# Kernel tuning notes

Measured on AMD Instinct MI355X. Metric: run time of the kernel, lower is better.

## Reference

```python
import jax, jax.numpy as jnp
import numpy as np

N_HEAD, DIM, D_K, D_V = 16, 1024, 64, 64
B, L = 4, 2048


def setup_inputs() -> dict:
    key = jax.random.key(0)
    ks = jax.random.split(key, 8)
    def xavier(k, shape, fan_in, fan_out):
        std = float(np.sqrt(2.0 / (fan_in + fan_out)))
        return jax.random.normal(k, shape, dtype=jnp.float32) * std
    return {
        "q": jax.random.normal(ks[0], (B, L, DIM), dtype=jnp.float32),
        "k": jax.random.normal(ks[1], (B, L, DIM), dtype=jnp.float32),
        "v": jax.random.normal(ks[2], (B, L, DIM), dtype=jnp.float32),
        "w_q": xavier(ks[3], (N_HEAD, DIM, D_K), DIM, D_K),
        "w_k": xavier(ks[4], (N_HEAD, DIM, D_K), DIM, D_K),
        "w_v": xavier(ks[5], (N_HEAD, DIM, D_V), DIM, D_V),
        "proj_w": xavier(ks[6], (DIM, N_HEAD * D_V), N_HEAD * D_V, DIM),
        "proj_b": jnp.zeros((DIM,), dtype=jnp.float32),
    }


def reference(q, k, v, w_q, w_k, w_v, proj_w, proj_b):
    batch, len_q, dim = q.shape
    # NOTE: original scales by sqrt(dim) (model dim), not sqrt(d_k)
    scale = jnp.asarray(np.sqrt(dim), dtype=q.dtype)
    # per-head projections: [h, b, q, dk]
    qh = jnp.einsum('bqd,hdk->hbqk', q, w_q)
    kh = jnp.einsum('bsd,hdk->hbsk', k, w_k)
    vh = jnp.einsum('bsd,hdv->hbsv', v, w_v)
    scores = jnp.einsum('hbqk,hbsk->hbqs', qh, kh) / scale
    attn = jax.nn.softmax(scores, axis=-1)
    out = jnp.einsum('hbqs,hbsv->hbqv', attn, vh)
    # concat heads along last dim: [b, q, h*dv] (head-major order, matching torch.cat(split))
    out = jnp.transpose(out, (1, 2, 0, 3)).reshape(batch, len_q, -1)
    # output projection (dropout is identity at eval)
    return out @ proj_w.T + proj_b
```

## Files before the change

kernel.cpp:

```cpp
#include <hip/hip_runtime.h>
#include <hip/hip_bf16.h>
#include <stdint.h>

#define NH 16
#define DM 1024
#define DKV 64
#define BB 4
#define LL 2048
#define MT (BB*LL)
#define NT (LL/64)

typedef __bf16 bf16;
typedef __bf16 bf16x8 __attribute__((ext_vector_type(8)));
typedef float f32x4 __attribute__((ext_vector_type(4)));
typedef float f32x16 __attribute__((ext_vector_type(16)));
typedef unsigned int u32x2 __attribute__((ext_vector_type(2)));
typedef unsigned int u32x4 __attribute__((ext_vector_type(4)));

__device__ __forceinline__ void gload_lds16(const void* g, void* l) {
  __builtin_amdgcn_global_load_lds(
      (const __attribute__((address_space(1))) unsigned int*)g,
      (__attribute__((address_space(3))) unsigned int*)l, 16, 0, 0);
}

__device__ __forceinline__ unsigned short bfbits(float x) {
  bf16 b = (bf16)x;
  return __builtin_bit_cast(unsigned short, b);
}

__device__ __forceinline__ float fast_exp2(float x) {
#if defined(__has_builtin)
#if __has_builtin(__builtin_amdgcn_exp2f)
  return __builtin_amdgcn_exp2f(x);
#else
  float r; asm("v_exp_f32 %0, %1" : "=v"(r) : "v"(x)); return r;
#endif
#else
  float r; asm("v_exp_f32 %0, %1" : "=v"(r) : "v"(x)); return r;
#endif
}

#if defined(__has_builtin)
#if __has_builtin(__builtin_amdgcn_permlane32_swap)
#define HAVE_PLSWAP 1
#endif
#endif

__device__ __forceinline__ u32x2 plswap(unsigned int a, unsigned int b, int hi) {
#ifdef HAVE_PLSWAP
  auto rr = __builtin_amdgcn_permlane32_swap(a, b, false, false);
  u32x2 r; r.x = rr[0]; r.y = rr[1];
  return r;
#else
  unsigned int pa = (unsigned int)__shfl_xor((int)a, 32);
  unsigned int pb_ = (unsigned int)__shfl_xor((int)b, 32);
  u32x2 r;
  r.x = hi ? pb_ : a;
  r.y = hi ? b : pa;
  return r;
#endif
}

__device__ __forceinline__ bf16x8 pack8(const f32x4& lo, const f32x4& hi2) {
  u32x4 u;
  u.x = (unsigned int)bfbits(lo[0]) | ((unsigned int)bfbits(lo[1]) << 16);
  u.y = (unsigned int)bfbits(lo[2]) | ((unsigned int)bfbits(lo[3]) << 16);
  u.z = (unsigned int)bfbits(hi2[0]) | ((unsigned int)bfbits(hi2[1]) << 16);
  u.w = (unsigned int)bfbits(hi2[2]) | ((unsigned int)bfbits(hi2[3]) << 16);
  return __builtin_bit_cast(bf16x8, u);
}

__global__ __launch_bounds__(256) void prep_w(const float* __restrict__ w0, const float* __restrict__ w1,
                                              const float* __restrict__ w2, const float* __restrict__ pw,
                                              bf16* __restrict__ o0, bf16* __restrict__ o1,
                                              bf16* __restrict__ o2, bf16* __restrict__ Wp) {
  __shared__ float t[64][65];
  if (blockIdx.z < 3) {
    const float* w = blockIdx.z == 0 ? w0 : (blockIdx.z == 1 ? w1 : w2);
    bf16* o = blockIdx.z == 0 ? o0 : (blockIdx.z == 1 ? o1 : o2);
    int h = blockIdx.y, d0 = blockIdx.x * 64;
    const float* src = w + ((size_t)h * DM + d0) * DKV;
    for (int i = threadIdx.x; i < 64 * 64; i += 256) {
      int r = i >> 6, c = i & 63;
      t[r][c] = src[(size_t)r * DKV + c];
    }
    __syncthreads();
    for (int i = threadIdx.x; i < 64 * 64; i += 256) {
      int kk = i >> 6, d = i & 63;
      o[((size_t)(h * 64 + kk)) * DM + d0 + d] = (bf16)t[d][kk];
    }
  } else {
    int base = ((blockIdx.y * 16 + blockIdx.x) * 256 + threadIdx.x) * 2;
#pragma unroll
    for (int e = 0; e < 2; ++e) {
      int i = base + e;
      const float4* p = (const float4*)pw + (size_t)i * 2;
      float4 a = p[0], b = p[1];
      bf16x8 r;
      r[0] = (bf16)a.x; r[1] = (bf16)a.y; r[2] = (bf16)a.z; r[3] = (bf16)a.w;
      r[4] = (bf16)b.x; r[5] = (bf16)b.y; r[6] = (bf16)b.z; r[7] = (bf16)b.w;
      *((bf16x8*)Wp + i) = r;
    }
  }
}

__global__ __launch_bounds__(256) void gemm_qkv(const float* __restrict__ Qf, const float* __restrict__ Kf,
                                                const float* __restrict__ Vf, const bf16* __restrict__ Wqt,
                                                const bf16* __restrict__ Wkt, const bf16* __restrict__ Wvt,
                                                bf16* __restrict__ QH, bf16* __restrict__ KH,
                                                bf16* __restrict__ VT) {
  __shared__ float sAf[128 * 64];
  __shared__ bf16 sB[128 * 64];
  const int bid = blockIdx.x;
  const int xcd = bid & 7;
  const int j   = bid >> 3;
  const int nb  = j & 7;
  const int t   = j >> 3;
  const int mb  = xcd + 8 * (t & 7);
  const int mode = t >> 3;
  const float* A = mode == 0 ? Qf : (mode == 1 ? Kf : Vf);
  const bf16* Bt = mode == 0 ? Wqt : (mode == 1 ? Wkt : Wvt);
  const int tid = threadIdx.x;
  const int w = tid >> 6, l = tid & 63;
  const int c = l & 15, g4 = l >> 4;
  const int wm = w >> 1, wn = w & 1;
  const int m0 = mb * 128, n0 = nb * 128;

  f32x4 acc[4][4] = {};
  for (int kt = 0; kt < 1024; kt += 64) {
#pragma unroll
    for (int jj = 0; jj < 8; ++jj) {
      int gi = jj * 256 + tid;
      int row = gi >> 4, slot = gi & 15;
      int sg = slot ^ (row & 15);
      gload_lds16(A + (size_t)(m0 + row) * 1024 + kt + sg * 4,
                  (char*)sAf + (jj * 256 + w * 64) * 16);
    }
#pragma unroll
    for (int i = 0; i < 4; ++i) {
      int blk = i * 4 + w;
      int row = blk * 8 + (l >> 3);
      int g = (l & 7) ^ (row & 7);
      gload_lds16(Bt + ((size_t)(n0 + row)) * 1024 + kt + g * 8, (char*)sB + blk * 1024);
    }
    __syncthreads();
#pragma unroll
    for (int ks = 0; ks < 2; ++ks) {
      bf16x8 af[4], bfr[4];
#pragma unroll
      for (int x = 0; x < 4; ++x) {
        int ar = wm * 64 + x * 16 + c;
        int p0 = ks * 8 + g4 * 2;
        int s0 = p0 ^ (ar & 15), s1 = (p0 + 1) ^ (ar & 15);
        f32x4 lo = *(const f32x4*)((const char*)sAf + ar * 256 + s0 * 16);
        f32x4 hi2 = *(const f32x4*)((const char*)sAf + ar * 256 + s1 * 16);
        af[x] = pack8(lo, hi2);
        int br = wn * 64 + x * 16 + c;
        bfr[x] = *(const bf16x8*)((const char*)sB + br * 128 + (((ks * 4 + g4) ^ (br & 7)) * 16));
      }
#pragma unroll
      for (int x = 0; x < 4; ++x)
#pragma unroll
        for (int y = 0; y < 4; ++y)
          acc[x][y] = __builtin_amdgcn_mfma_f32_16x16x32_bf16(af[x], bfr[y], acc[x][y], 0, 0, 0);
    }
    __syncthreads();
  }

  const int mm = m0 + wm * 64, nn = n0 + wn * 64;
  if (mode < 2) {
    bf16* O = mode == 0 ? QH : KH;
    const float s = (mode == 0) ? 0.03125f * 1.44269504088896f : 1.0f;
#pragma unroll
    for (int x = 0; x < 4; ++x)
#pragma unroll
      for (int y = 0; y < 4; ++y)
#pragma unroll
        for (int r = 0; r < 4; ++r) {
          int m = mm + x * 16 + g4 * 4 + r;
          int n = nn + y * 16 + c;
          O[(size_t)m * 1024 + n] = (bf16)(acc[x][y][r] * s);
        }
  } else {
    bf16* O = VT;
#pragma unroll
    for (int x = 0; x < 4; ++x)
#pragma unroll
      for (int y = 0; y < 4; ++y) {
        int mb2 = mm + x * 16 + g4 * 4;
        int n = nn + y * 16 + c;
        int bb2 = mb2 >> 11, sidx = mb2 & 2047;
        int hh2 = n >> 6, dv = n & 63;
        unsigned int u0 = bfbits(acc[x][y][0]) | ((unsigned int)bfbits(acc[x][y][1]) << 16);
        unsigned int u1 = bfbits(acc[x][y][2]) | ((unsigned int)bfbits(acc[x][y][3]) << 16);
        *(uint2*)(O + ((size_t)((hh2 * 4 + bb2) * 64 + dv)) * LL + sidx) = make_uint2(u0, u1);
      }
  }
}

__global__ __launch_bounds__(256) void gemm_proj(const bf16* __restrict__ A, const bf16* __restrict__ Bt,
                                                 float* __restrict__ Out, const float* __restrict__ bias) {
  __shared__ bf16 sA[128 * 64];
  __shared__ bf16 sB[128 * 64];
  const int tid = threadIdx.x;
  const int w = tid >> 6, l = tid & 63;
  const int c = l & 15, g4 = l >> 4;
  const int wm = w >> 1, wn = w & 1;
  const int m0 = blockIdx.y * 128, n0 = blockIdx.x * 128;

  f32x4 acc[4][4] = {};
  for (int kt = 0; kt < 1024; kt += 64) {
#pragma unroll
    for (int i = 0; i < 4; ++i) {
      int blk = i * 4 + w;
      int row = blk * 8 + (l >> 3);
      int g = (l & 7) ^ (row & 7);
      gload_lds16(A + ((size_t)(m0 + row)) * 1024 + kt + g * 8, (char*)sA + blk * 1024);
      gload_lds16(Bt + ((size_t)(n0 + row)) * 1024 + kt + g * 8, (char*)sB + blk * 1024);
    }
    __syncthreads();
#pragma unroll
    for (int ks = 0; ks < 2; ++ks) {
      bf16x8 af[4], bfr[4];
#pragma unroll
      for (int x = 0; x < 4; ++x) {
        int ar = wm * 64 + x * 16 + c;
        af[x] = *(const bf16x8*)((const char*)sA + ar * 128 + (((ks * 4 + g4) ^ (ar & 7)) * 16));
        int br = wn * 64 + x * 16 + c;
        bfr[x] = *(const bf16x8*)((const char*)sB + br * 128 + (((ks * 4 + g4) ^ (br & 7)) * 16));
      }
#pragma unroll
      for (int x = 0; x < 4; ++x)
#pragma unroll
        for (int y = 0; y < 4; ++y)
          acc[x][y] = __builtin_amdgcn_mfma_f32_16x16x32_bf16(af[x], bfr[y], acc[x][y], 0, 0, 0);
    }
    __syncthreads();
  }

  const int mm = m0 + wm * 64, nn = n0 + wn * 64;
#pragma unroll
  for (int x = 0; x < 4; ++x)
#pragma unroll
    for (int y = 0; y < 4; ++y)
#pragma unroll
      for (int r = 0; r < 4; ++r) {
        int m = mm + x * 16 + g4 * 4 + r;
        int n = nn + y * 16 + c;
        Out[(size_t)m * 1024 + n] = acc[x][y][r] + bias[n];
      }
}

__global__ __launch_bounds__(256, 2) void attn_kernel(const bf16* __restrict__ qh,
                                                      const bf16* __restrict__ kh,
                                                      const bf16* __restrict__ vt,
                                                      bf16* __restrict__ o) {
  __shared__ bf16 sK[4][64 * 64];
  __shared__ bf16 sV[4][64 * 64];
  const int tid = threadIdx.x, w = tid >> 6, l = tid & 63;
  const int c = l & 31, hi = l >> 5;
  const int bh = blockIdx.x, b = bh & 3, h = bh >> 2;
  const int q0 = blockIdx.y * 256 + w * 64;

  const bf16* qbase = qh + ((size_t)(b * LL)) * DM + h * 64;
  const bf16* kbase = kh + ((size_t)(b * LL)) * DM + h * 64;
  const bf16* vbase = vt + ((size_t)((h * 4 + b) * 64)) * LL;

  bf16x8 qfA[4], qfB[4];
#pragma unroll
  for (int ks = 0; ks < 4; ++ks) {
    qfA[ks] = *(const bf16x8*)(qbase + (size_t)(q0 + c) * DM + ks * 16 + hi * 8);
    qfB[ks] = *(const bf16x8*)(qbase + (size_t)(q0 + 32 + c) * DM + ks * 16 + hi * 8);
  }

  bf16x8 onesf;
#pragma unroll
  for (int i = 0; i < 8; ++i) onesf[i] = (bf16)1.0f;

  f32x16 oA0 = {}, oA1 = {}, oB0 = {}, oB1 = {};
  f32x16 lAa = {}, lBa = {};

  auto STAGE = [&](int bufi, int kv0) {
#pragma unroll
    for (int j = 0; j < 2; ++j) {
      int gi = w * 128 + j * 64 + l;
      int row = gi >> 3;
      int g = (gi & 7) ^ (row & 7);
      gload_lds16(kbase + (size_t)(kv0 + row) * DM + g * 8,
                  (char*)sK[bufi] + (w * 128 + j * 64) * 16);
      gload_lds16(vbase + (size_t)row * LL + kv0 + g * 8,
                  (char*)sV[bufi] + (w * 128 + j * 64) * 16);
    }
  };

  auto EXPPACK = [&](f32x16& st0, f32x16& st1, bf16x8* pb) {
#pragma unroll
    for (int r = 0; r < 16; ++r) st0[r] = fast_exp2(st0[r]);
#pragma unroll
    for (int r = 0; r < 16; ++r) st1[r] = fast_exp2(st1[r]);
#pragma unroll
    for (int t = 0; t < 2; ++t) {
      const f32x16& st = t ? st1 : st0;
      unsigned int u[4][2];
#pragma unroll
      for (int g2 = 0; g2 < 4; ++g2) {
        u[g2][0] = (unsigned int)bfbits(st[4 * g2 + 0]) | ((unsigned int)bfbits(st[4 * g2 + 1]) << 16);
        u[g2][1] = (unsigned int)bfbits(st[4 * g2 + 2]) | ((unsigned int)bfbits(st[4 * g2 + 3]) << 16);
      }
      u32x2 s0 = plswap(u[0][0], u[1][0], hi);
      u32x2 s1 = plswap(u[0][1], u[1][1], hi);
      u32x4 w0; w0.x = s0.x; w0.y = s1.x; w0.z = s0.y; w0.w = s1.y;
      pb[2 * t] = __builtin_bit_cast(bf16x8, w0);
      u32x2 s2 = plswap(u[2][0], u[3][0], hi);
      u32x2 s3 = plswap(u[2][1], u[3][1], hi);
      u32x4 w1; w1.x = s2.x; w1.y = s3.x; w1.z = s2.y; w1.w = s3.y;
      pb[2 * t + 1] = __builtin_bit_cast(bf16x8, w1);
    }
  };

  auto TILE = [&](int bufi) {
    const char* Kb = (const char*)sK[bufi];
    const char* Vb = (const char*)sV[bufi];

    bf16x8 kf[8];
#pragma unroll
    for (int ks = 0; ks < 4; ++ks) {
      int slot = ((ks * 2 + hi) ^ (c & 7)) * 16;
      kf[ks]     = *(const bf16x8*)(Kb + c * 128 + slot);
      kf[4 + ks] = *(const bf16x8*)(Kb + (32 + c) * 128 + slot);
    }
    f32x16 sA0 = {}, sA1 = {}, sB0 = {}, sB1 = {};
    __builtin_amdgcn_s_setprio(1);
#pragma unroll
    for (int ks = 0; ks < 4; ++ks) {
      sA0 = __builtin_amdgcn_mfma_f32_32x32x16_bf16(kf[ks],     qfA[ks], sA0, 0, 0, 0);
      sA1 = __builtin_amdgcn_mfma_f32_32x32x16_bf16(kf[4 + ks], qfA[ks], sA1, 0, 0, 0);
    }
#pragma unroll
    for (int ks = 0; ks < 4; ++ks) {
      sB0 = __builtin_amdgcn_mfma_f32_32x32x16_bf16(kf[ks],     qfB[ks], sB0, 0, 0, 0);
      sB1 = __builtin_amdgcn_mfma_f32_32x32x16_bf16(kf[4 + ks], qfB[ks], sB1, 0, 0, 0);
    }
    __builtin_amdgcn_s_setprio(0);

    bf16x8 pbA[4];
    EXPPACK(sA0, sA1, pbA);

    bf16x8 vf[8];
#pragma unroll
    for (int ks = 0; ks < 4; ++ks) {
      int slot = ((ks * 2 + hi) ^ (c & 7)) * 16;
      vf[ks]     = *(const bf16x8*)(Vb + c * 128 + slot);
      vf[4 + ks] = *(const bf16x8*)(Vb + (32 + c) * 128 + slot);
    }
    __builtin_amdgcn_s_setprio(1);
#pragma unroll
    for (int ks = 0; ks < 4; ++ks) {
      oA0 = __builtin_amdgcn_mfma_f32_32x32x16_bf16(vf[ks],     pbA[ks], oA0, 0, 0, 0);
      oA1 = __builtin_amdgcn_mfma_f32_32x32x16_bf16(vf[4 + ks], pbA[ks], oA1, 0, 0, 0);
      lAa = __builtin_amdgcn_mfma_f32_32x32x16_bf16(onesf,      pbA[ks], lAa, 0, 0, 0);
    }
    __builtin_amdgcn_s_setprio(0);

    bf16x8 pbB[4];
    EXPPACK(sB0, sB1, pbB);
    __builtin_amdgcn_s_setprio(1);
#pragma unroll
    for (int ks = 0; ks < 4; ++ks) {
      oB0 = __builtin_amdgcn_mfma_f32_32x32x16_bf16(vf[ks],     pbB[ks], oB0, 0, 0, 0);
      oB1 = __builtin_amdgcn_mfma_f32_32x32x16_bf16(vf[4 + ks], pbB[ks], oB1, 0, 0, 0);
      lBa = __builtin_amdgcn_mfma_f32_32x32x16_bf16(onesf,      pbB[ks], lBa, 0, 0, 0);
    }
    __builtin_amdgcn_s_setprio(0);
  };

  STAGE(0, 0);
  STAGE(1, 64);

  for (int wd = 0; wd < 16; ++wd) {
    __builtin_amdgcn_s_barrier();
    int t2 = 2 * wd + 2;
    if (t2 < NT) {
      STAGE(t2 & 3, t2 * 64);
      STAGE((t2 + 1) & 3, (t2 + 1) * 64);
      asm volatile("s_waitcnt vmcnt(8)" ::: "memory");
    } else {
      asm volatile("s_waitcnt vmcnt(0)" ::: "memory");
    }
    TILE((2 * wd) & 3);
    TILE((2 * wd + 1) & 3);
  }

  bf16* ob = o + ((size_t)(b * LL)) * DM + h * 64;
  {
    float inv = 1.0f / lAa[0];
#pragma unroll
    for (int dt = 0; dt < 2; ++dt) {
      const f32x16& oc = dt ? oA1 : oA0;
#pragma unroll
      for (int rg = 0; rg < 4; ++rg) {
        int dv0 = dt * 32 + rg * 8 + hi * 4;
        unsigned int u0 = (unsigned int)bfbits(oc[rg * 4 + 0] * inv) |
                          ((unsigned int)bfbits(oc[rg * 4 + 1] * inv) << 16);
        unsigned int u1 = (unsigned int)bfbits(oc[rg * 4 + 2] * inv) |
                          ((unsigned int)bfbits(oc[rg * 4 + 3] * inv) << 16);
        *(uint2*)(ob + (size_t)(q0 + c) * DM + dv0) = make_uint2(u0, u1);
      }
    }
  }
  {
    float inv = 1.0f / lBa[0];
#pragma unroll
    for (int dt = 0; dt < 2; ++dt) {
      const f32x16& oc = dt ? oB1 : oB0;
#pragma unroll
      for (int rg = 0; rg < 4; ++rg) {
        int dv0 = dt * 32 + rg * 8 + hi * 4;
        unsigned int u0 = (unsigned int)bfbits(oc[rg * 4 + 0] * inv) |
                          ((unsigned int)bfbits(oc[rg * 4 + 1] * inv) << 16);
        unsigned int u1 = (unsigned int)bfbits(oc[rg * 4 + 2] * inv) |
                          ((unsigned int)bfbits(oc[rg * 4 + 3] * inv) << 16);
        *(uint2*)(ob + (size_t)(q0 + 32 + c) * DM + dv0) = make_uint2(u0, u1);
      }
    }
  }
}

extern "C" void kernel_launch(void* const* d_in, const int* in_sizes, int n_in,
                              void* d_out, int out_size, void* d_ws, size_t ws_size,
                              hipStream_t stream) {
  const float* q  = (const float*)d_in[0];
  const float* k  = (const float*)d_in[1];
  const float* v  = (const float*)d_in[2];
  const float* wq = (const float*)d_in[3];
  const float* wk = (const float*)d_in[4];
  const float* wv = (const float*)d_in[5];
  const float* pw = (const float*)d_in[6];
  const float* pb = (const float*)d_in[7];
  float* out = (float*)d_out;

  char* ws = (char*)d_ws;
  const size_t SX = (size_t)MT * DM * 2;
  const size_t SW = (size_t)DM * DM * 2;
  bf16* Wqt = (bf16*)(ws);
  bf16* Wkt = (bf16*)(ws + SW);
  bf16* Wvt = (bf16*)(ws + 2 * SW);
  bf16* Wp  = (bf16*)(ws + 3 * SW);
  bf16* QH  = (bf16*)(ws + 4 * SW);
  bf16* KH  = (bf16*)(ws + 4 * SW + SX);
  bf16* VT  = (bf16*)(ws + 4 * SW + 2 * SX);
  bf16* OO  = (bf16*)(ws + 4 * SW + 3 * SX);

  prep_w<<<dim3(16, 16, 4), 256, 0, stream>>>(wq, wk, wv, pw, Wqt, Wkt, Wvt, Wp);

  gemm_qkv<<<dim3(1536), 256, 0, stream>>>(q, k, v, Wqt, Wkt, Wvt, QH, KH, VT);

  attn_kernel<<<dim3(64, 8), 256, 0, stream>>>(QH, KH, VT, OO);

  gemm_proj<<<dim3(8, 64), 256, 0, stream>>>(OO, Wp, out, pb);
}
```

Before: 208.5 us.

## Register-prefetch QKV GEMM tiles, convert A to bf16 before LDS, remap proj blocks

```diff
diff --git a/kernel.cpp b/kernel.cpp
--- a/kernel.cpp
+++ b/kernel.cpp
@@ -109,7 +109,7 @@
                                                 const bf16* __restrict__ Wkt, const bf16* __restrict__ Wvt,
                                                 bf16* __restrict__ QH, bf16* __restrict__ KH,
                                                 bf16* __restrict__ VT) {
-  __shared__ float sAf[128 * 64];
+  __shared__ bf16 sA[128 * 64];
   __shared__ bf16 sB[128 * 64];
   const int bid = blockIdx.x;
   const int xcd = bid & 7;
@@ -126,45 +126,64 @@
   const int wm = w >> 1, wn = w & 1;
   const int m0 = mb * 128, n0 = nb * 128;
 
+  int grow[4], gsg[4];
+#pragma unroll
+  for (int jj = 0; jj < 4; ++jj) {
+    int gi = jj * 256 + tid;
+    grow[jj] = gi >> 3;
+    gsg[jj] = (gi & 7) ^ (grow[jj] & 7);
+  }
+
+  f32x4 ra[4][2];
+  u32x4 rbr[4];
+
+  auto LOADA = [&](int kt) {
+#pragma unroll
+    for (int jj = 0; jj < 4; ++jj) {
+      const float* s = A + (size_t)(m0 + grow[jj]) * 1024 + kt + gsg[jj] * 8;
+      ra[jj][0] = *(const f32x4*)s;
+      ra[jj][1] = *(const f32x4*)(s + 4);
+    }
+  };
+  auto LOADB = [&](int kt) {
+#pragma unroll
+    for (int jj = 0; jj < 4; ++jj)
+      rbr[jj] = *(const u32x4*)(Bt + (size_t)(n0 + grow[jj]) * 1024 + kt + gsg[jj] * 8);
+  };
+  auto WRITE = [&]() {
+#pragma unroll
+    for (int jj = 0; jj < 4; ++jj) {
+      *(bf16x8*)((char*)sA + (jj * 256 + tid) * 16) = pack8(ra[jj][0], ra[jj][1]);
+      *(u32x4*)((char*)sB + (jj * 256 + tid) * 16) = rbr[jj];
+    }
+  };
+
   f32x4 acc[4][4] = {};
-  for (int kt = 0; kt < 1024; kt += 64) {
-#pragma unroll
-    for (int jj = 0; jj < 8; ++jj) {
-      int gi = jj * 256 + tid;
-      int row = gi >> 4, slot = gi & 15;
-      int sg = slot ^ (row & 15);
-      gload_lds16(A + (size_t)(m0 + row) * 1024 + kt + sg * 4,
-                  (char*)sAf + (jj * 256 + w * 64) * 16);
-    }
-#pragma unroll
-    for (int i = 0; i < 4; ++i) {
-      int blk = i * 4 + w;
-      int row = blk * 8 + (l >> 3);
-      int g = (l & 7) ^ (row & 7);
-      gload_lds16(Bt + ((size_t)(n0 + row)) * 1024 + kt + g * 8, (char*)sB + blk * 1024);
-    }
-    __syncthreads();
+  LOADA(0); LOADB(0);
+  for (int it = 0; it < 16; ++it) {
+    WRITE();
+    if (it < 15) { LOADA((it + 1) * 64); LOADB((it + 1) * 64); }
+    asm volatile("s_waitcnt lgkmcnt(0)" ::: "memory");
+    __builtin_amdgcn_s_barrier();
 #pragma unroll
     for (int ks = 0; ks < 2; ++ks) {
       bf16x8 af[4], bfr[4];
 #pragma unroll
       for (int x = 0; x < 4; ++x) {
         int ar = wm * 64 + x * 16 + c;
-        int p0 = ks * 8 + g4 * 2;
-        int s0 = p0 ^ (ar & 15), s1 = (p0 + 1) ^ (ar & 15);
-        f32x4 lo = *(const f32x4*)((const char*)sAf + ar * 256 + s0 * 16);
-        f32x4 hi2 = *(const f32x4*)((const char*)sAf + ar * 256 + s1 * 16);
-        af[x] = pack8(lo, hi2);
+        af[x] = *(const bf16x8*)((const char*)sA + ar * 128 + (((ks * 4 + g4) ^ (ar & 7)) * 16));
         int br = wn * 64 + x * 16 + c;
         bfr[x] = *(const bf16x8*)((const char*)sB + br * 128 + (((ks * 4 + g4) ^ (br & 7)) * 16));
       }
+      __builtin_amdgcn_s_setprio(1);
 #pragma unroll
       for (int x = 0; x < 4; ++x)
 #pragma unroll
         for (int y = 0; y < 4; ++y)
           acc[x][y] = __builtin_amdgcn_mfma_f32_16x16x32_bf16(af[x], bfr[y], acc[x][y], 0, 0, 0);
-    }
-    __syncthreads();
+      __builtin_amdgcn_s_setprio(0);
+    }
+    __builtin_amdgcn_s_barrier();
   }
 
   const int mm = m0 + wm * 64, nn = n0 + wn * 64;
@@ -202,11 +221,16 @@
                                                  float* __restrict__ Out, const float* __restrict__ bias) {
   __shared__ bf16 sA[128 * 64];
   __shared__ bf16 sB[128 * 64];
+  const int bid = blockIdx.x;
+  const int xcd = bid & 7;
+  const int j = bid >> 3;
+  const int nb = j & 7;
+  const int mb = xcd + 8 * (j >> 3);
   const int tid = threadIdx.x;
   const int w = tid >> 6, l = tid & 63;
   const int c = l & 15, g4 = l >> 4;
   const int wm = w >> 1, wn = w & 1;
-  const int m0 = blockIdx.y * 128, n0 = blockIdx.x * 128;
+  const int m0 = mb * 128, n0 = nb * 128;
 
   f32x4 acc[4][4] = {};
   for (int kt = 0; kt < 1024; kt += 64) {
@@ -457,5 +481,5 @@
 
   attn_kernel<<<dim3(64, 8), 256, 0, stream>>>(QH, KH, VT, OO);
 
-  gemm_proj<<<dim3(8, 64), 256, 0, stream>>>(OO, Wp, out, pb);
-}
+  gemm_proj<<<dim3(512), 256, 0, stream>>>(OO, Wp, out, pb);
+}
```

After: 197.7 us (median of 2 runs). -5.2%, faster.
